# Performance work log

Hardware: AMD Instinct MI355X
Metric: run time of the kernel (lower is better)

## Reference

```python
import jax, jax.numpy as jnp
import numpy as np

NEG = -1e32
EPS_LN = 1e-5

def _layer_norm(x, w, b):
    mu = jnp.mean(x, axis=-1, keepdims=True)
    var = jnp.mean((x - mu) ** 2, axis=-1, keepdims=True)
    return (x - mu) / jnp.sqrt(var + EPS_LN) * w + b

def setup_inputs() -> dict:
    key = jax.random.key(0)
    ks = jax.random.split(key, 10)
    B, S, D, H, F = 2, 2048, 1024, 16, 4096
    s = 0.02
    return {
        "query": jax.random.normal(ks[0], (B, S, D), jnp.float32),
        "key": jax.random.normal(ks[1], (B, S, D), jnp.float32),
        "values": jax.random.normal(ks[2], (B, S, D), jnp.float32),
        "Wk": jax.random.normal(ks[3], (D, D), jnp.float32) * s,
        "bk": jnp.zeros((D,), jnp.float32),
        "Wv": jax.random.normal(ks[4], (D, D), jnp.float32) * s,
        "bv": jnp.zeros((D,), jnp.float32),
        "Wo": jax.random.normal(ks[5], (D, D), jnp.float32) * s,
        "bo": jnp.zeros((D,), jnp.float32),
        "gammas": jax.random.normal(ks[6], (H, 1, 1), jnp.float32),
        "ln1_w": jnp.ones((D,), jnp.float32),
        "ln1_b": jnp.zeros((D,), jnp.float32),
        "W1": jax.random.normal(ks[7], (F, D), jnp.float32) * s,
        "b1": jnp.zeros((F,), jnp.float32),
        "W2": jax.random.normal(ks[8], (D, F), jnp.float32) * s,
        "b2": jnp.zeros((D,), jnp.float32),
        "ln2_w": jnp.ones((D,), jnp.float32),
        "ln2_b": jnp.zeros((D,), jnp.float32),
        "mask": 1,
    }

def _forward(query, key, values, Wk, bk, Wv, bv, Wo, bo, gammas,
             ln1_w, ln1_b, W1, b1, W2, b2, ln2_w, ln2_b, mask):
    B, S, D = query.shape
    H = gammas.shape[0]
    dk = D // H
    # kq_same=True: q and k both use k_linear
    def proj(x, W, b):
        return (x @ W.T + b).reshape(B, S, H, dk).transpose(0, 2, 1, 3)  # bhsd
    q = proj(query, Wk, bk)
    k = proj(key, Wk, bk)
    v = proj(values, Wv, bv)

    scores = jnp.einsum("bhqd,bhkd->bhqk", q, k) / np.sqrt(dk).astype(np.float32)
    # src_mask: np.triu(ones, k=mask)==0 -> allowed where j <= i + mask - 1
    allow = jnp.tril(jnp.ones((S, S), bool), k=mask - 1)[None, None]  # (1,1,S,S)

    # --- distance decay (no_grad block in torch) ---
    scores_ = jax.nn.softmax(jnp.where(allow, scores, NEG), axis=-1)
    scores_ = scores_ * allow.astype(scores_.dtype)
    distcum = jnp.cumsum(scores_, axis=-1)
    disttotal = jnp.sum(scores_, axis=-1, keepdims=True)
    idx = jnp.arange(S)
    position_effect = jnp.abs(idx[:, None] - idx[None, :]).astype(jnp.float32)[None, None]
    dist_scores = jnp.sqrt(jnp.clip((disttotal - distcum) * position_effect, 0.0, None))
    gamma = -jax.nn.softplus(gammas)[None]  # (1,H,1,1)
    total_effect = jnp.clip(jnp.exp(dist_scores * gamma), 1e-5, 1e5)
    total_effect = jax.lax.stop_gradient(total_effect)
    # ---

    scores = scores * total_effect
    scores = jnp.where(allow, scores, NEG)
    attn = jax.nn.softmax(scores, axis=-1)
    out = jnp.einsum("bhqk,bhkd->bhqd", attn, v)
    concat = out.transpose(0, 2, 1, 3).reshape(B, S, D)
    query2 = concat @ Wo.T + bo

    x = _layer_norm(query + query2, ln1_w, ln1_b)
    ff = jax.nn.relu(x @ W1.T + b1) @ W2.T + b2
    x = _layer_norm(x + ff, ln2_w, ln2_b)
    return x

def reference(query, key, values, Wk, bk, Wv, bv, Wo, bo, gammas,
              ln1_w, ln1_b, W1, b1, W2, b2, ln2_w, ln2_b, mask):
    return _forward(query, key, values, Wk, bk, Wv, bv, Wo, bo, gammas,
                    ln1_w, ln1_b, W1, b1, W2, b2, ln2_w, ln2_b, mask)
```

## Files before the change

### kernel.cpp

```cpp
#include <hip/hip_runtime.h>
#include <hip/hip_bf16.h>

#define B_   2
#define S_   2048
#define D_   1024
#define H_   16
#define DK_  64
#define F_   4096
#define M_   (B_*S_)
#define PD   72

typedef __attribute__((ext_vector_type(8))) short short8;
typedef __attribute__((ext_vector_type(4))) float f32x4;

__device__ __forceinline__ float bf2f(unsigned short s) { return __uint_as_float(((unsigned int)s) << 16); }
__device__ __forceinline__ unsigned short f2bf(float f) {
    unsigned int u = __float_as_uint(f);
    u += 0x7fffu + ((u >> 16) & 1u);
    return (unsigned short)(u >> 16);
}

__device__ __forceinline__ bool probe_f32(const unsigned int* p) {
    return *p == 0x3F800000u;
}
__device__ __forceinline__ float ld1e(const void* p, size_t idx, bool f32) {
    return f32 ? ((const float*)p)[idx] : bf2f(((const unsigned short*)p)[idx]);
}
__device__ __forceinline__ void st1e(void* p, size_t idx, bool f32, float v) {
    if (f32) ((float*)p)[idx] = v;
    else     ((unsigned short*)p)[idx] = f2bf(v);
}

__device__ __forceinline__ void async16(void* lds, const void* g) {
    __builtin_amdgcn_global_load_lds(
        (const __attribute__((address_space(1))) void*)g,
        (__attribute__((address_space(3))) void*)lds, 16, 0, 0);
}

template <bool IS_MAX>
__device__ __forceinline__ float block_reduce(float val, float* buf, int tid) {
    buf[tid] = val;
    __syncthreads();
    #pragma unroll
    for (int off = 128; off > 0; off >>= 1) {
        if (tid < off) {
            float o = buf[tid + off];
            buf[tid] = IS_MAX ? fmaxf(buf[tid], o) : (buf[tid] + o);
        }
        __syncthreads();
    }
    float r = buf[0];
    __syncthreads();
    return r;
}

__global__ __launch_bounds__(256) void cvt_all(
    const void* __restrict__ W1, const void* __restrict__ W2,
    const void* __restrict__ Wk, const void* __restrict__ Wv,
    const void* __restrict__ Wo,
    unsigned short* __restrict__ W1b, unsigned short* __restrict__ W2b,
    unsigned short* __restrict__ Wkb, unsigned short* __restrict__ Wvb,
    unsigned short* __restrict__ Wob,
    const unsigned int* __restrict__ probe)
{
    const bool p32 = probe_f32(probe);
    const int blk = blockIdx.x;
    const void* src;
    unsigned short* dst;
    int off;
    if (blk < 2048)      { src = W1; dst = W1b; off = blk; }
    else if (blk < 4096) { src = W2; dst = W2b; off = blk - 2048; }
    else if (blk < 4608) { src = Wk; dst = Wkb; off = blk - 4096; }
    else if (blk < 5120) { src = Wv; dst = Wvb; off = blk - 4608; }
    else                 { src = Wo; dst = Wob; off = blk - 5120; }
    const int i8 = (off * 256 + threadIdx.x) * 8;
    if (p32) {
        const float4 a = *(const float4*)((const float*)src + i8);
        const float4 b = *(const float4*)((const float*)src + i8 + 4);
        short8 o;
        o[0] = (short)f2bf(a.x); o[1] = (short)f2bf(a.y);
        o[2] = (short)f2bf(a.z); o[3] = (short)f2bf(a.w);
        o[4] = (short)f2bf(b.x); o[5] = (short)f2bf(b.y);
        o[6] = (short)f2bf(b.z); o[7] = (short)f2bf(b.w);
        *(short8*)(dst + i8) = o;
    } else {
        *(uint4*)(dst + i8) = *(const uint4*)((const unsigned short*)src + i8);
    }
}

template <int RELU, int AEXT, int CEXT>
__device__ __forceinline__ void gemm_body(
    const void* __restrict__ A,
    const unsigned short* __restrict__ W,
    const void* __restrict__ bias,
    void* __restrict__ C,
    int M, int N, int K, bool p32, int bx, int by)
{
    __shared__ unsigned short As[128 * 32];
    __shared__ unsigned short Ws[128 * 32];

    const bool a32 = AEXT && p32;
    const bool c32 = CEXT && p32;

    const int tid = threadIdx.x;
    const int lane = tid & 63;
    const int w = tid >> 6;
    const int wr = w >> 1;
    const int wc = w & 1;
    const int col16 = lane & 15;
    const int quad = lane >> 4;

    const int m0 = by * 128;
    const int n0 = bx * 128;

    const int c0 = tid, c1 = 256 + tid;
    const int r0 = c0 >> 2, kc0 = (c0 & 3) * 8;
    const int r1 = c1 >> 2, kc1 = (c1 & 3) * 8;

    f32x4 acc[4][4];
    #pragma unroll
    for (int mt = 0; mt < 4; mt++)
        #pragma unroll
        for (int nt = 0; nt < 4; nt++)
            acc[mt][nt] = (f32x4){0.f, 0.f, 0.f, 0.f};

    for (int k0 = 0; k0 < K; k0 += 32) {
        __syncthreads();
        async16(&Ws[c0 * 8], W + (size_t)(n0 + r0) * K + k0 + kc0);
        async16(&Ws[c1 * 8], W + (size_t)(n0 + r1) * K + k0 + kc1);
        if (a32) {
            const float* a0 = (const float*)A + (size_t)(m0 + r0) * K + k0 + kc0;
            const float* a1 = (const float*)A + (size_t)(m0 + r1) * K + k0 + kc1;
            const float4 x0 = *(const float4*)a0, y0 = *(const float4*)(a0 + 4);
            const float4 x1 = *(const float4*)a1, y1 = *(const float4*)(a1 + 4);
            short8 s0, s1;
            s0[0] = (short)f2bf(x0.x); s0[1] = (short)f2bf(x0.y);
            s0[2] = (short)f2bf(x0.z); s0[3] = (short)f2bf(x0.w);
            s0[4] = (short)f2bf(y0.x); s0[5] = (short)f2bf(y0.y);
            s0[6] = (short)f2bf(y0.z); s0[7] = (short)f2bf(y0.w);
            s1[0] = (short)f2bf(x1.x); s1[1] = (short)f2bf(x1.y);
            s1[2] = (short)f2bf(x1.z); s1[3] = (short)f2bf(x1.w);
            s1[4] = (short)f2bf(y1.x); s1[5] = (short)f2bf(y1.y);
            s1[6] = (short)f2bf(y1.z); s1[7] = (short)f2bf(y1.w);
            *(short8*)&As[c0 * 8] = s0;
            *(short8*)&As[c1 * 8] = s1;
        } else {
            const unsigned short* Ab = (const unsigned short*)A;
            async16(&As[c0 * 8], Ab + (size_t)(m0 + r0) * K + k0 + kc0);
            async16(&As[c1 * 8], Ab + (size_t)(m0 + r1) * K + k0 + kc1);
        }
        __syncthreads();

        short8 av[4], bv[4];
        #pragma unroll
        for (int mt = 0; mt < 4; mt++)
            av[mt] = *(const short8*)&As[(wr * 64 + mt * 16 + col16) * 32 + quad * 8];
        #pragma unroll
        for (int nt = 0; nt < 4; nt++)
            bv[nt] = *(const short8*)&Ws[(wc * 64 + nt * 16 + col16) * 32 + quad * 8];
        #pragma unroll
        for (int mt = 0; mt < 4; mt++)
            #pragma unroll
            for (int nt = 0; nt < 4; nt++)
                acc[mt][nt] = __builtin_amdgcn_mfma_f32_16x16x32_bf16(
                    av[mt], bv[nt], acc[mt][nt], 0, 0, 0);
    }

    #pragma unroll
    for (int mt = 0; mt < 4; mt++) {
        const int row = m0 + wr * 64 + mt * 16 + quad * 4;
        #pragma unroll
        for (int nt = 0; nt < 4; nt++) {
            const int col = n0 + wc * 64 + nt * 16 + col16;
            const float bb = ld1e(bias, col, p32);
            #pragma unroll
            for (int r = 0; r < 4; r++) {
                float v = acc[mt][nt][r] + bb;
                if (RELU) v = fmaxf(v, 0.f);
                st1e(C, (size_t)(row + r) * N + col, c32, v);
            }
        }
    }
}

template <int RELU, int AEXT, int CEXT>
__global__ __launch_bounds__(256) void gemm_mf(
    const void* __restrict__ A,
    const unsigned short* __restrict__ W,
    const void* __restrict__ bias,
    void* __restrict__ C,
    int M, int N, int K,
    const unsigned int* __restrict__ probe)
{
    gemm_body<RELU, AEXT, CEXT>(A, W, bias, C, M, N, K, probe_f32(probe),
                                blockIdx.x, blockIdx.y);
}

__global__ __launch_bounds__(256) void gemm_proj(
    const void* __restrict__ A0, const void* __restrict__ A1, const void* __restrict__ A2,
    const unsigned short* __restrict__ Wkb, const unsigned short* __restrict__ Wvb,
    const void* __restrict__ bk, const void* __restrict__ bv,
    unsigned short* __restrict__ qw, unsigned short* __restrict__ kw,
    unsigned short* __restrict__ vw,
    const unsigned int* __restrict__ probe)
{
    const int z = blockIdx.z;
    const void* A = (z == 0) ? A0 : (z == 1) ? A1 : A2;
    const unsigned short* W = (z == 2) ? Wvb : Wkb;
    const void* bias = (z == 2) ? bv : bk;
    void* C = (z == 0) ? (void*)qw : (z == 1) ? (void*)kw : (void*)vw;
    gemm_body<0, 1, 0>(A, W, bias, C, M_, D_, D_, probe_f32(probe),
                       blockIdx.x, blockIdx.y);
}

__global__ __launch_bounds__(256) void attn_mfma(
    const unsigned short* __restrict__ qw,
    const unsigned short* __restrict__ kw,
    const unsigned short* __restrict__ vw,
    const void* __restrict__ gam,
    const int* __restrict__ maskp,
    unsigned short* __restrict__ outc,
    const unsigned int* __restrict__ probe)
{
    __shared__ unsigned short Qs[64 * PD];
    __shared__ unsigned short Ks[64 * PD];
    __shared__ unsigned short Vt[64 * PD];
    __shared__ float mtS[64 * 33];
    __shared__ float ctS[64 * 33];
    __shared__ float m1S[64];
    __shared__ float rT1S[64];
    unsigned int* const Pu = (unsigned int*)Qs;

    const bool p32 = probe_f32(probe);
    const int tid = threadIdx.x;
    const int lane = tid & 63;
    const int w = tid >> 6;
    const int col16 = lane & 15;
    const int quad = lane >> 4;
    const int bid = blockIdx.x;
    const int qt = 31 - (bid >> 5);
    const int bh = bid & 31;
    const int h = bh & 15;
    const int b = bh >> 4;
    const int i0 = qt * 64;

    const int mask = *maskp;
    long long nje = (long long)i0 + 63 + (long long)mask;
    int njmax = (nje > S_) ? S_ : (int)nje;
    if (njmax < 1) njmax = 1;
    const int ntiles = (njmax + 63) >> 6;

    const float L2E = 1.44269504088896f;
    const float gval = ld1e(gam, h, p32);
    const float sp = (gval > 20.f) ? gval : log1pf(__expf(gval));
    const float g2 = -sp * L2E;
    const float SC2 = 0.125f * L2E;

    const int myrow = i0 + w * 16 + col16;

    #pragma unroll
    for (int cc = 0; cc < 2; cc++) {
        const int c = tid + cc * 256;
        const int row = c >> 3, dc = c & 7;
        const uint4 u = *(const uint4*)(qw + (size_t)(b * S_ + i0 + row) * D_ + h * 64 + dc * 8);
        *(uint4*)&Qs[row * PD + dc * 8] = u;
    }
    __syncthreads();

    short8 avq[2];
    #pragma unroll
    for (int ks = 0; ks < 2; ks++)
        avq[ks] = *(const short8*)&Qs[(w * 16 + col16) * PD + ks * 32 + quad * 8];

    for (int t = 0; t < ntiles; t++) {
        const int j0 = t * 64;
        __syncthreads();
        #pragma unroll
        for (int cc = 0; cc < 2; cc++) {
            const int c = tid + cc * 256;
            const int row = c >> 3, dc = c & 7;
            const uint4 u = *(const uint4*)(kw + (size_t)(b * S_ + j0 + row) * D_ + h * 64 + dc * 8);
            *(uint4*)&Ks[row * PD + dc * 8] = u;
        }
        __syncthreads();

        f32x4 acc[4];
        #pragma unroll
        for (int nt = 0; nt < 4; nt++) acc[nt] = (f32x4){0.f, 0.f, 0.f, 0.f};
        #pragma unroll
        for (int ks = 0; ks < 2; ks++)
            #pragma unroll
            for (int nt = 0; nt < 4; nt++) {
                const short8 kv = *(const short8*)&Ks[(nt * 16 + col16) * PD + ks * 32 + quad * 8];
                acc[nt] = __builtin_amdgcn_mfma_f32_16x16x32_bf16(kv, avq[ks], acc[nt], 0, 0, 0);
            }

        float lm = -3.0e38f;
        #pragma unroll
        for (int nt = 0; nt < 4; nt++)
            #pragma unroll
            for (int r = 0; r < 4; r++) {
                const int j = j0 + nt * 16 + quad * 4 + r;
                const bool al = j < myrow + mask;
                const float s2 = acc[nt][r] * SC2;
                lm = al ? fmaxf(lm, s2) : lm;
            }
        lm = fmaxf(lm, __shfl_xor(lm, 16, 64));
        lm = fmaxf(lm, __shfl_xor(lm, 32, 64));

        float cs = 0.f;
        #pragma unroll
        for (int nt = 0; nt < 4; nt++)
            #pragma unroll
            for (int r = 0; r < 4; r++) {
                const int j = j0 + nt * 16 + quad * 4 + r;
                const bool al = j < myrow + mask;
                cs += al ? __builtin_amdgcn_exp2f(acc[nt][r] * SC2 - lm) : 0.f;
            }
        cs += __shfl_xor(cs, 16, 64);
        cs += __shfl_xor(cs, 32, 64);

        if (lane < 16) {
            const int row = w * 16 + lane;
            mtS[row * 33 + t] = lm;
            ctS[row * 33 + t] = cs;
        }
    }

    __syncthreads();
    if (lane < 16) {
        const int row = w * 16 + lane;
        float m1v = -3.0e38f;
        for (int t = 0; t < ntiles; t++) m1v = fmaxf(m1v, mtS[row * 33 + t]);
        float runv = 0.f;
        for (int t = 0; t < ntiles; t++) {
            const float e = ctS[row * 33 + t] * __builtin_amdgcn_exp2f(mtS[row * 33 + t] - m1v);
            ctS[row * 33 + t] = runv;
            runv += e;
        }
        m1S[row] = m1v;
        rT1S[row] = 1.0f / runv;
    }
    __syncthreads();

    const float m1 = m1S[w * 16 + col16];
    const float rT1 = rT1S[w * 16 + col16];

    float m2 = -3.0e38f;
    float l2 = 0.f;
    f32x4 O[4];
    #pragma unroll
    for (int nt = 0; nt < 4; nt++) O[nt] = (f32x4){0.f, 0.f, 0.f, 0.f};

    for (int t = 0; t < ntiles; t++) {
        const int j0 = t * 64;
        __syncthreads();
        #pragma unroll
        for (int cc = 0; cc < 2; cc++) {
            const int c = tid + cc * 256;
            const int row = c >> 3, dc = c & 7;
            const uint4 u = *(const uint4*)(kw + (size_t)(b * S_ + j0 + row) * D_ + h * 64 + dc * 8);
            *(uint4*)&Ks[row * PD + dc * 8] = u;
        }
        #pragma unroll
        for (int cc = 0; cc < 2; cc++) {
            const int dc = w + cc * 4;
            const int key = lane;
            const uint4 u = *(const uint4*)(vw + (size_t)(b * S_ + j0 + key) * D_ + h * 64 + dc * 8);
            unsigned short* dst = &Vt[(dc * 8) * PD + key];
            dst[0 * PD] = (unsigned short)(u.x & 0xffff);
            dst[1 * PD] = (unsigned short)(u.x >> 16);
            dst[2 * PD] = (unsigned short)(u.y & 0xffff);
            dst[3 * PD] = (unsigned short)(u.y >> 16);
            dst[4 * PD] = (unsigned short)(u.z & 0xffff);
            dst[5 * PD] = (unsigned short)(u.z >> 16);
            dst[6 * PD] = (unsigned short)(u.w & 0xffff);
            dst[7 * PD] = (unsigned short)(u.w >> 16);
        }
        __syncthreads();

        f32x4 acc[4];
        #pragma unroll
        for (int nt = 0; nt < 4; nt++) acc[nt] = (f32x4){0.f, 0.f, 0.f, 0.f};
        #pragma unroll
        for (int ks = 0; ks < 2; ks++)
            #pragma unroll
            for (int nt = 0; nt < 4; nt++) {
                const short8 kv = *(const short8*)&Ks[(nt * 16 + col16) * PD + ks * 32 + quad * 8];
                acc[nt] = __builtin_amdgcn_mfma_f32_16x16x32_bf16(kv, avq[ks], acc[nt], 0, 0, 0);
            }

        const float pref = ctS[(w * 16 + col16) * 33 + t];

        float tv[4][4];
        float base = 0.f;
        #pragma unroll
        for (int nt = 0; nt < 4; nt++) {
            float ev[4], loc[4];
            float run = 0.f;
            #pragma unroll
            for (int r = 0; r < 4; r++) {
                const int j = j0 + nt * 16 + quad * 4 + r;
                const bool al = j < myrow + mask;
                ev[r] = al ? __builtin_amdgcn_exp2f(acc[nt][r] * SC2 - m1) : 0.f;
                run += ev[r];
                loc[r] = run;
            }
            float v = run;
            const float u1 = __shfl_up(v, 16, 64); if (quad >= 1) v += u1;
            const float u2 = __shfl_up(v, 32, 64); if (quad >= 2) v += u2;
            const float excl = v - run;
            const float ntsum = __shfl(v, col16 + 48, 64);
            #pragma unroll
            for (int r = 0; r < 4; r++) {
                const int j = j0 + nt * 16 + quad * 4 + r;
                const bool al = j < myrow + mask;
                const float cumn = (pref + base + excl + loc[r]) * rT1;
                const float rem = fmaxf(1.f - cumn, 0.f);
                const float pe = fabsf((float)(myrow - j));
                float te = __builtin_amdgcn_exp2f(g2 * sqrtf(rem * pe));
                te = fminf(fmaxf(te, 1e-5f), 1e5f);
                tv[nt][r] = al ? (acc[nt][r] * SC2) * te : -3.0e38f;
            }
            base += ntsum;
        }

        float tm = -3.0e38f;
        #pragma unroll
        for (int nt = 0; nt < 4; nt++)
            #pragma unroll
            for (int r = 0; r < 4; r++)
                tm = fmaxf(tm, tv[nt][r]);
        tm = fmaxf(tm, __shfl_xor(tm, 16, 64));
        tm = fmaxf(tm, __shfl_xor(tm, 32, 64));

        const float mnew = fmaxf(m2, tm);
        const float alpha = __builtin_amdgcn_exp2f(m2 - mnew);
        m2 = mnew;
        l2 *= alpha;
        #pragma unroll
        for (int r = 0; r < 4; r++) {
            const float aO = __shfl(alpha, quad * 4 + r, 64);
            #pragma unroll
            for (int nt = 0; nt < 4; nt++) O[nt][r] *= aO;
        }

        float lsum = 0.f;
        #pragma unroll
        for (int nt = 0; nt < 4; nt++) {
            float p0 = __builtin_amdgcn_exp2f(tv[nt][0] - m2);
            float p1 = __builtin_amdgcn_exp2f(tv[nt][1] - m2);
            float p2 = __builtin_amdgcn_exp2f(tv[nt][2] - m2);
            float p3 = __builtin_amdgcn_exp2f(tv[nt][3] - m2);
            lsum += (p0 + p1) + (p2 + p3);
            uint2 pk;
            pk.x = ((unsigned int)f2bf(p1) << 16) | f2bf(p0);
            pk.y = ((unsigned int)f2bf(p3) << 16) | f2bf(p2);
            *(uint2*)&Pu[(w * 16 + col16) * 36 + nt * 8 + quad * 2] = pk;
        }
        lsum += __shfl_xor(lsum, 16, 64);
        lsum += __shfl_xor(lsum, 32, 64);
        l2 += lsum;

        const short8 pa0 = *(const short8*)&Pu[(w * 16 + col16) * 36 + 0 * 16 + quad * 4];
        const short8 pa1 = *(const short8*)&Pu[(w * 16 + col16) * 36 + 1 * 16 + quad * 4];
        #pragma unroll
        for (int nt = 0; nt < 4; nt++) {
            const short8 bv0 = *(const short8*)&Vt[(nt * 16 + col16) * PD + 0 * 32 + quad * 8];
            const short8 bv1 = *(const short8*)&Vt[(nt * 16 + col16) * PD + 1 * 32 + quad * 8];
            O[nt] = __builtin_amdgcn_mfma_f32_16x16x32_bf16(pa0, bv0, O[nt], 0, 0, 0);
            O[nt] = __builtin_amdgcn_mfma_f32_16x16x32_bf16(pa1, bv1, O[nt], 0, 0, 0);
        }
    }

    const float rl2 = 1.0f / l2;
    float rl2O[4];
    #pragma unroll
    for (int r = 0; r < 4; r++) rl2O[r] = __shfl(rl2, quad * 4 + r, 64);
    #pragma unroll
    for (int nt = 0; nt < 4; nt++)
        #pragma unroll
        for (int r = 0; r < 4; r++)
            outc[(size_t)(b * S_ + i0 + w * 16 + quad * 4 + r) * D_ + h * 64 + nt * 16 + col16] =
                f2bf(O[nt][r] * rl2O[r]);
}

__global__ __launch_bounds__(256) void ln_fused(
    const void* __restrict__ A,
    const void* __restrict__ Bq,
    const void* __restrict__ w,
    const void* __restrict__ bias,
    void* __restrict__ out,
    const unsigned int* __restrict__ probe, int aext, int bext, int oext)
{
    __shared__ float xs[D_];
    __shared__ float red[256];
    const bool p32 = probe_f32(probe);
    const bool a32 = aext && p32;
    const bool b32 = bext && p32;
    const bool o32 = oext && p32;

    const int tid = threadIdx.x;
    const size_t row = (size_t)blockIdx.x * D_;

    float lsum = 0.f;
    #pragma unroll
    for (int qq = 0; qq < 4; qq++) {
        const int j = tid + qq * 256;
        const float x = ld1e(A, row + j, a32) + ld1e(Bq, row + j, b32);
        xs[j] = x;
        lsum += x;
    }
    const float mu = block_reduce<false>(lsum, red, tid) * (1.0f / D_);

    float lv = 0.f;
    #pragma unroll
    for (int qq = 0; qq < 4; qq++) {
        const int j = tid + qq * 256;
        const float dd = xs[j] - mu;
        lv += dd * dd;
    }
    const float var = block_reduce<false>(lv, red, tid) * (1.0f / D_);
    const float rs = rsqrtf(var + 1e-5f);

    #pragma unroll
    for (int qq = 0; qq < 4; qq++) {
        const int j = tid + qq * 256;
        const float o = (xs[j] - mu) * rs * ld1e(w, j, p32) + ld1e(bias, j, p32);
        st1e(out, row + j, o32, o);
    }
}

extern "C" void kernel_launch(void* const* d_in, const int* in_sizes, int n_in,
                              void* d_out, int out_size, void* d_ws, size_t ws_size,
                              hipStream_t stream)
{
    (void)in_sizes; (void)n_in; (void)out_size; (void)ws_size;

    const void* query  = d_in[0];
    const void* key_   = d_in[1];
    const void* values = d_in[2];
    const void* Wk     = d_in[3];
    const void* bk     = d_in[4];
    const void* Wv     = d_in[5];
    const void* bv     = d_in[6];
    const void* Wo     = d_in[7];
    const void* bo     = d_in[8];
    const void* gammas = d_in[9];
    const void* ln1w   = d_in[10];
    const void* ln1b   = d_in[11];
    const void* W1     = d_in[12];
    const void* b1     = d_in[13];
    const void* W2     = d_in[14];
    const void* b2     = d_in[15];
    const void* ln2w   = d_in[16];
    const void* ln2b   = d_in[17];
    const int*  maskp  = (const int*)d_in[18];
    const unsigned int* probe = (const unsigned int*)ln1w;

    char* ws = (char*)d_ws;
    const size_t MiB = 1024 * 1024;
    unsigned short* W1b = (unsigned short*)(ws + 0 * MiB);
    unsigned short* W2b = (unsigned short*)(ws + 8 * MiB);
    unsigned short* Wkb = (unsigned short*)(ws + 16 * MiB);
    unsigned short* Wvb = (unsigned short*)(ws + 18 * MiB);
    unsigned short* Wob = (unsigned short*)(ws + 20 * MiB);
    unsigned short* qw  = (unsigned short*)(ws + 22 * MiB);
    unsigned short* kw  = (unsigned short*)(ws + 30 * MiB);
    unsigned short* vw  = (unsigned short*)(ws + 38 * MiB);
    unsigned short* cw  = (unsigned short*)(ws + 46 * MiB);
    unsigned short* x1  = (unsigned short*)(ws + 22 * MiB);
    unsigned short* fh  = (unsigned short*)(ws + 30 * MiB);

    const dim3 blk(256);
    cvt_all<<<dim3(5632), blk, 0, stream>>>(W1, W2, Wk, Wv, Wo,
                                            W1b, W2b, Wkb, Wvb, Wob, probe);
    gemm_proj<<<dim3(D_ / 128, M_ / 128, 3), blk, 0, stream>>>(
        query, key_, values, Wkb, Wvb, bk, bv, qw, kw, vw, probe);
    attn_mfma<<<dim3(B_ * H_ * (S_ / 64)), blk, 0, stream>>>(
        qw, kw, vw, gammas, maskp, cw, probe);
    gemm_mf<0, 0, 0><<<dim3(D_ / 128, M_ / 128), blk, 0, stream>>>(
        cw, Wob, bo, x1, M_, D_, D_, probe);
    ln_fused<<<dim3(M_), blk, 0, stream>>>(query, x1, ln1w, ln1b, x1, probe, 1, 0, 0);
    gemm_mf<1, 0, 0><<<dim3(F_ / 128, M_ / 128), blk, 0, stream>>>(
        x1, W1b, b1, fh, M_, F_, D_, probe);
    gemm_mf<0, 0, 1><<<dim3(D_ / 128, M_ / 128), blk, 0, stream>>>(
        fh, W2b, b2, d_out, M_, D_, F_, probe);
    ln_fused<<<dim3(M_), blk, 0, stream>>>(x1, d_out, ln2w, ln2b, d_out, probe, 0, 1, 1);
}
```

Baseline: 546.3 us.

## Pre-transpose V, skip masking on full tiles, use fixed softmax max bound

Adds a separate kernel that writes V transposed per head, so the attention kernel loads V tiles with vector copies instead of scattered 2-byte LDS stores. The attention kernel now applies the causal mask only on tiles that are not fully visible. It also drops the online-softmax rescaling by using a fixed upper bound max(m1,0) for the second softmax, which is valid because the decay factor is at most 1. The row sum is reduced once at the end, and packing uses the hardware bf16 pack instruction. In exchange it costs an extra launch and a full V round trip through global memory, and it relies on the bound to keep exponents from overflowing.

```diff
diff --git a/kernel.cpp b/kernel.cpp
--- a/kernel.cpp
+++ b/kernel.cpp
@@ -35,6 +35,12 @@
     __builtin_amdgcn_global_load_lds(
         (const __attribute__((address_space(1))) void*)g,
         (__attribute__((address_space(3))) void*)lds, 16, 0, 0);
+}
+
+__device__ __forceinline__ unsigned int cvt_pk_bf16(float a, float b) {
+    unsigned int r;
+    asm("v_cvt_pk_bf16_f32 %0, %1, %2" : "=v"(r) : "v"(a), "v"(b));
+    return r;
 }
 
 template <bool IS_MAX>
@@ -213,10 +219,45 @@
                        blockIdx.x, blockIdx.y);
 }
 
+__global__ __launch_bounds__(256) void vtrans(
+    const unsigned short* __restrict__ vw,
+    unsigned short* __restrict__ vtg)
+{
+    __shared__ unsigned short T[64 * PD];
+    const int tid = threadIdx.x;
+    const int bid = blockIdx.x;
+    const int bh = bid & 31;
+    const int kt = bid >> 5;
+    const int h = bh & 15, b = bh >> 4;
+    #pragma unroll
+    for (int cc = 0; cc < 2; cc++) {
+        const int c = tid + cc * 256;
+        const int key = c >> 3, dc = c & 7;
+        const uint4 u = *(const uint4*)(vw + (size_t)(b * S_ + kt * 64 + key) * D_ + h * 64 + dc * 8);
+        unsigned short* dst = &T[(dc * 8) * PD + key];
+        dst[0 * PD] = (unsigned short)(u.x & 0xffff);
+        dst[1 * PD] = (unsigned short)(u.x >> 16);
+        dst[2 * PD] = (unsigned short)(u.y & 0xffff);
+        dst[3 * PD] = (unsigned short)(u.y >> 16);
+        dst[4 * PD] = (unsigned short)(u.z & 0xffff);
+        dst[5 * PD] = (unsigned short)(u.z >> 16);
+        dst[6 * PD] = (unsigned short)(u.w & 0xffff);
+        dst[7 * PD] = (unsigned short)(u.w >> 16);
+    }
+    __syncthreads();
+    #pragma unroll
+    for (int cc = 0; cc < 2; cc++) {
+        const int c = tid + cc * 256;
+        const int d = c >> 3, kc = c & 7;
+        const uint4 u = *(const uint4*)&T[d * PD + kc * 8];
+        *(uint4*)(vtg + ((size_t)bh * 64 + d) * S_ + kt * 64 + kc * 8) = u;
+    }
+}
+
 __global__ __launch_bounds__(256) void attn_mfma(
     const unsigned short* __restrict__ qw,
     const unsigned short* __restrict__ kw,
-    const unsigned short* __restrict__ vw,
+    const unsigned short* __restrict__ vtg,
     const void* __restrict__ gam,
     const int* __restrict__ maskp,
     unsigned short* __restrict__ outc,
@@ -249,6 +290,12 @@
     int njmax = (nje > S_) ? S_ : (int)nje;
     if (njmax < 1) njmax = 1;
     const int ntiles = (njmax + 63) >> 6;
+    long long fm = (long long)i0 + (long long)mask - 64;
+    int nfull = 0;
+    if (fm >= 0) {
+        long long v = (fm >> 6) + 1;
+        nfull = (v > ntiles) ? ntiles : (int)v;
+    }
 
     const float L2E = 1.44269504088896f;
     const float gval = ld1e(gam, h, p32);
@@ -257,6 +304,7 @@
     const float SC2 = 0.125f * L2E;
 
     const int myrow = i0 + w * 16 + col16;
+    const int limq = myrow + mask - quad * 4;
 
     #pragma unroll
     for (int cc = 0; cc < 2; cc++) {
@@ -295,28 +343,32 @@
                 acc[nt] = __builtin_amdgcn_mfma_f32_16x16x32_bf16(kv, avq[ks], acc[nt], 0, 0, 0);
             }
 
-        float lm = -3.0e38f;
+        if (t >= nfull) {
+            #pragma unroll
+            for (int nt = 0; nt < 4; nt++) {
+                const int Ln = limq - j0 - nt * 16;
+                #pragma unroll
+                for (int r = 0; r < 4; r++)
+                    acc[nt][r] = (r < Ln) ? acc[nt][r] : -3.0e38f;
+            }
+        }
+
+        float am = -3.0e38f;
         #pragma unroll
         for (int nt = 0; nt < 4; nt++)
             #pragma unroll
-            for (int r = 0; r < 4; r++) {
-                const int j = j0 + nt * 16 + quad * 4 + r;
-                const bool al = j < myrow + mask;
-                const float s2 = acc[nt][r] * SC2;
-                lm = al ? fmaxf(lm, s2) : lm;
-            }
-        lm = fmaxf(lm, __shfl_xor(lm, 16, 64));
-        lm = fmaxf(lm, __shfl_xor(lm, 32, 64));
+            for (int r = 0; r < 4; r++)
+                am = fmaxf(am, acc[nt][r]);
+        am = fmaxf(am, __shfl_xor(am, 16, 64));
+        am = fmaxf(am, __shfl_xor(am, 32, 64));
+        const float lm = fmaxf(am * SC2, -1.0e30f);
 
         float cs = 0.f;
         #pragma unroll
         for (int nt = 0; nt < 4; nt++)
             #pragma unroll
-            for (int r = 0; r < 4; r++) {
-                const int j = j0 + nt * 16 + quad * 4 + r;
-                const bool al = j < myrow + mask;
-                cs += al ? __builtin_amdgcn_exp2f(acc[nt][r] * SC2 - lm) : 0.f;
-            }
+            for (int r = 0; r < 4; r++)
+                cs += __builtin_amdgcn_exp2f(__builtin_fmaf(acc[nt][r], SC2, -lm));
         cs += __shfl_xor(cs, 16, 64);
         cs += __shfl_xor(cs, 32, 64);
 
@@ -345,8 +397,8 @@
 
     const float m1 = m1S[w * 16 + col16];
     const float rT1 = rT1S[w * 16 + col16];
-
-    float m2 = -3.0e38f;
+    const float m2s = fmaxf(m1, 0.f);
+
     float l2 = 0.f;
     f32x4 O[4];
     #pragma unroll
@@ -364,18 +416,10 @@
         }
         #pragma unroll
         for (int cc = 0; cc < 2; cc++) {
-            const int dc = w + cc * 4;
-            const int key = lane;
-            const uint4 u = *(const uint4*)(vw + (size_t)(b * S_ + j0 + key) * D_ + h * 64 + dc * 8);
-            unsigned short* dst = &Vt[(dc * 8) * PD + key];
-            dst[0 * PD] = (unsigned short)(u.x & 0xffff);
-            dst[1 * PD] = (unsigned short)(u.x >> 16);
-            dst[2 * PD] = (unsigned short)(u.y & 0xffff);
-            dst[3 * PD] = (unsigned short)(u.y >> 16);
-            dst[4 * PD] = (unsigned short)(u.z & 0xffff);
-            dst[5 * PD] = (unsigned short)(u.z >> 16);
-            dst[6 * PD] = (unsigned short)(u.w & 0xffff);
-            dst[7 * PD] = (unsigned short)(u.w >> 16);
+            const int c = tid + cc * 256;
+            const int d = c >> 3, kc = c & 7;
+            const uint4 u = *(const uint4*)(vtg + ((size_t)bh * 64 + d) * S_ + j0 + kc * 8);
+            *(uint4*)&Vt[d * PD + kc * 8] = u;
         }
         __syncthreads();
 
@@ -390,77 +434,61 @@
                 acc[nt] = __builtin_amdgcn_mfma_f32_16x16x32_bf16(kv, avq[ks], acc[nt], 0, 0, 0);
             }
 
-        const float pref = ctS[(w * 16 + col16) * 33 + t];
-
-        float tv[4][4];
-        float base = 0.f;
+        if (t >= nfull) {
+            #pragma unroll
+            for (int nt = 0; nt < 4; nt++) {
+                const int Ln = limq - j0 - nt * 16;
+                #pragma unroll
+                for (int r = 0; r < 4; r++)
+                    acc[nt][r] = (r < Ln) ? acc[nt][r] : -3.0e38f;
+            }
+        }
+
+        float loc[4][4], run[4];
         #pragma unroll
         for (int nt = 0; nt < 4; nt++) {
-            float ev[4], loc[4];
-            float run = 0.f;
+            float rr = 0.f;
             #pragma unroll
             for (int r = 0; r < 4; r++) {
-                const int j = j0 + nt * 16 + quad * 4 + r;
-                const bool al = j < myrow + mask;
-                ev[r] = al ? __builtin_amdgcn_exp2f(acc[nt][r] * SC2 - m1) : 0.f;
-                run += ev[r];
-                loc[r] = run;
+                rr += __builtin_amdgcn_exp2f(__builtin_fmaf(acc[nt][r], SC2, -m1));
+                loc[nt][r] = rr;
             }
-            float v = run;
+            run[nt] = rr;
+        }
+        float excl[4], tot[4];
+        #pragma unroll
+        for (int nt = 0; nt < 4; nt++) {
+            float v = run[nt];
             const float u1 = __shfl_up(v, 16, 64); if (quad >= 1) v += u1;
             const float u2 = __shfl_up(v, 32, 64); if (quad >= 2) v += u2;
-            const float excl = v - run;
-            const float ntsum = __shfl(v, col16 + 48, 64);
+            excl[nt] = v - run[nt];
+            tot[nt] = __shfl(v, col16 + 48, 64);
+        }
+
+        const float pref = ctS[(w * 16 + col16) * 33 + t];
+        float Cb = pref;
+        #pragma unroll
+        for (int nt = 0; nt < 4; nt++) {
+            const float CeR = (Cb + excl[nt]) * rT1;
+            const float d0f = (float)(myrow - j0 - nt * 16 - quad * 4);
+            float p4[4];
             #pragma unroll
             for (int r = 0; r < 4; r++) {
-                const int j = j0 + nt * 16 + quad * 4 + r;
-                const bool al = j < myrow + mask;
-                const float cumn = (pref + base + excl + loc[r]) * rT1;
+                const float cumn = __builtin_fmaf(loc[nt][r], rT1, CeR);
                 const float rem = fmaxf(1.f - cumn, 0.f);
-                const float pe = fabsf((float)(myrow - j));
-                float te = __builtin_amdgcn_exp2f(g2 * sqrtf(rem * pe));
-                te = fminf(fmaxf(te, 1e-5f), 1e5f);
-                tv[nt][r] = al ? (acc[nt][r] * SC2) * te : -3.0e38f;
+                const float pe = fabsf(d0f - (float)r);
+                const float te = fmaxf(
+                    __builtin_amdgcn_exp2f(g2 * __builtin_amdgcn_sqrtf(rem * pe)), 1e-5f);
+                const float tv = (acc[nt][r] * SC2) * te;
+                p4[r] = __builtin_amdgcn_exp2f(tv - m2s);
+                l2 += p4[r];
             }
-            base += ntsum;
-        }
-
-        float tm = -3.0e38f;
-        #pragma unroll
-        for (int nt = 0; nt < 4; nt++)
-            #pragma unroll
-            for (int r = 0; r < 4; r++)
-                tm = fmaxf(tm, tv[nt][r]);
-        tm = fmaxf(tm, __shfl_xor(tm, 16, 64));
-        tm = fmaxf(tm, __shfl_xor(tm, 32, 64));
-
-        const float mnew = fmaxf(m2, tm);
-        const float alpha = __builtin_amdgcn_exp2f(m2 - mnew);
-        m2 = mnew;
-        l2 *= alpha;
-        #pragma unroll
-        for (int r = 0; r < 4; r++) {
-            const float aO = __shfl(alpha, quad * 4 + r, 64);
-            #pragma unroll
-            for (int nt = 0; nt < 4; nt++) O[nt][r] *= aO;
-        }
-
-        float lsum = 0.f;
-        #pragma unroll
-        for (int nt = 0; nt < 4; nt++) {
-            float p0 = __builtin_amdgcn_exp2f(tv[nt][0] - m2);
-            float p1 = __builtin_amdgcn_exp2f(tv[nt][1] - m2);
-            float p2 = __builtin_amdgcn_exp2f(tv[nt][2] - m2);
-            float p3 = __builtin_amdgcn_exp2f(tv[nt][3] - m2);
-            lsum += (p0 + p1) + (p2 + p3);
             uint2 pk;
-            pk.x = ((unsigned int)f2bf(p1) << 16) | f2bf(p0);
-            pk.y = ((unsigned int)f2bf(p3) << 16) | f2bf(p2);
+            pk.x = cvt_pk_bf16(p4[0], p4[1]);
+            pk.y = cvt_pk_bf16(p4[2], p4[3]);
             *(uint2*)&Pu[(w * 16 + col16) * 36 + nt * 8 + quad * 2] = pk;
-        }
-        lsum += __shfl_xor(lsum, 16, 64);
-        lsum += __shfl_xor(lsum, 32, 64);
-        l2 += lsum;
+            Cb += tot[nt];
+        }
 
         const short8 pa0 = *(const short8*)&Pu[(w * 16 + col16) * 36 + 0 * 16 + quad * 4];
         const short8 pa1 = *(const short8*)&Pu[(w * 16 + col16) * 36 + 1 * 16 + quad * 4];
@@ -473,6 +501,8 @@
         }
     }
 
+    l2 += __shfl_xor(l2, 16, 64);
+    l2 += __shfl_xor(l2, 32, 64);
     const float rl2 = 1.0f / l2;
     float rl2O[4];
     #pragma unroll
@@ -569,6 +599,7 @@
     unsigned short* kw  = (unsigned short*)(ws + 30 * MiB);
     unsigned short* vw  = (unsigned short*)(ws + 38 * MiB);
     unsigned short* cw  = (unsigned short*)(ws + 46 * MiB);
+    unsigned short* vtg = (unsigned short*)(ws + 54 * MiB);
     unsigned short* x1  = (unsigned short*)(ws + 22 * MiB);
     unsigned short* fh  = (unsigned short*)(ws + 30 * MiB);
 
@@ -577,8 +608,9 @@
                                             W1b, W2b, Wkb, Wvb, Wob, probe);
     gemm_proj<<<dim3(D_ / 128, M_ / 128, 3), blk, 0, stream>>>(
         query, key_, values, Wkb, Wvb, bk, bv, qw, kw, vw, probe);
+    vtrans<<<dim3(1024), blk, 0, stream>>>(vw, vtg);
     attn_mfma<<<dim3(B_ * H_ * (S_ / 64)), blk, 0, stream>>>(
-        qw, kw, vw, gammas, maskp, cw, probe);
+        qw, kw, vtg, gammas, maskp, cw, probe);
     gemm_mf<0, 0, 0><<<dim3(D_ / 128, M_ / 128), blk, 0, stream>>>(
         cw, Wob, bo, x1, M_, D_, D_, probe);
     ln_fused<<<dim3(M_), blk, 0, stream>>>(query, x1, ln1w, ln1b, x1, probe, 1, 0, 0);
```

Measured after the change: 497.2 us. -9.0%, faster.
